# Kernel tuning notes

Measured on AMD Instinct MI355X. Metric: run time of the kernel, lower is better.

## Reference

```python
import jax, jax.numpy as jnp
import numpy as np

N_NODES = 100000
N_EDGES = 1600000
N_GRAPHS = 256
IN_DIM, HID, OUT_DIM = 20, 128, 30954


def setup_inputs() -> dict:
    key = jax.random.key(0)
    ks = jax.random.split(key, 9)
    x = jax.random.normal(ks[0], (N_NODES, IN_DIM), dtype=jnp.float32)
    edge_index = jax.random.randint(ks[1], (2, N_EDGES), 0, N_NODES, dtype=jnp.int64)
    batch = jnp.sort(jax.random.randint(ks[2], (N_NODES,), 0, N_GRAPHS, dtype=jnp.int64))
    s = 0.05
    W1 = jax.random.normal(ks[3], (IN_DIM, HID), dtype=jnp.float32) * s
    b1 = jax.random.normal(ks[4], (HID,), dtype=jnp.float32) * s
    W2 = jax.random.normal(ks[5], (HID, HID), dtype=jnp.float32) * s
    b2 = jax.random.normal(ks[6], (HID,), dtype=jnp.float32) * s
    Wc = jax.random.normal(ks[7], (HID, OUT_DIM), dtype=jnp.float32) * s
    bc = jax.random.normal(ks[8], (OUT_DIM,), dtype=jnp.float32) * s
    return {"x": x, "edge_index": edge_index, "batch": batch,
            "W1": W1, "b1": b1, "W2": W2, "b2": b2, "Wc": Wc, "bc": bc}


def _gcn_norm(edge_index, n_nodes):
    # add self loops (PyG GCNConv default), symmetric normalization
    loops = jnp.arange(n_nodes, dtype=edge_index.dtype)
    src = jnp.concatenate([edge_index[0], loops])
    dst = jnp.concatenate([edge_index[1], loops])
    deg = jax.ops.segment_sum(jnp.ones_like(dst, dtype=jnp.float32), dst,
                              num_segments=n_nodes)
    dinv = jnp.where(deg > 0, jax.lax.rsqrt(deg), 0.0)
    norm = dinv[src] * dinv[dst]  # [E+N]
    return src, dst, norm


def _gcn_conv(x, src, dst, norm, W, b, n_nodes):
    h = x @ W                              # [N, out] transform first (fewer msg flops)
    msg = h[src] * norm[:, None]           # gather + scale
    out = jax.ops.segment_sum(msg, dst, num_segments=n_nodes)
    return out + b


def reference(x, edge_index, batch, W1, b1, W2, b2, Wc, bc):
    n = x.shape[0]
    src, dst, norm = _gcn_norm(edge_index, n)
    h = jax.nn.relu(_gcn_conv(x, src, dst, norm, W1, b1, n))
    # dropout is identity in eval mode
    h = jax.nn.relu(_gcn_conv(h, src, dst, norm, W2, b2, n))
    # global mean pool per graph
    sums = jax.ops.segment_sum(h, batch, num_segments=N_GRAPHS)       # [G, HID]
    cnts = jax.ops.segment_sum(jnp.ones((n,), jnp.float32), batch,
                               num_segments=N_GRAPHS)
    pooled = sums / jnp.maximum(cnts, 1.0)[:, None]
    return pooled @ Wc + bc  # [G, OUT_DIM]
```

## Files before the change

kernel.cpp:

```cpp
#include <hip/hip_runtime.h>

#define HID 128
#define SCAN_B 256

__device__ __forceinline__ float bf_lo(unsigned int u) { return __uint_as_float(u << 16); }
__device__ __forceinline__ float bf_hi(unsigned int u) { return __uint_as_float(u & 0xFFFF0000u); }
__device__ __forceinline__ unsigned short f2bf(float f) {
    unsigned int u = __float_as_uint(f);
    unsigned int r = (u + 0x7FFFu + ((u >> 16) & 1u)) >> 16;
    return (unsigned short)r;
}

__global__ void detect_kernel(const unsigned int* __restrict__ p, int* __restrict__ flag) {
    if (threadIdx.x == 0 && blockIdx.x == 0) {
        int is64 = 1;
        for (int i = 0; i < 64; ++i) {
            if (p[2 * i + 1] != 0u) { is64 = 0; break; }
        }
        *flag = is64;
    }
}

__global__ void cvtdeg_kernel(const void* __restrict__ p, int* __restrict__ out,
                              int* __restrict__ deg, int E, const int* __restrict__ flag) {
    int i = blockIdx.x * blockDim.x + threadIdx.x;
    if (i < 2 * E) {
        int v = (*flag) ? (int)((const long long*)p)[i] : ((const int*)p)[i];
        out[i] = v;
        if (i >= E) atomicAdd(&deg[v], 1);
    }
}

__global__ void zero_kernel(float4* __restrict__ p, long long n4) {
    long long i = (long long)blockIdx.x * blockDim.x + threadIdx.x;
    long long stride = (long long)gridDim.x * blockDim.x;
    for (; i < n4; i += stride) p[i] = make_float4(0.f, 0.f, 0.f, 0.f);
}

__global__ void cvtx_kernel(const float* __restrict__ x, unsigned short* __restrict__ xb, int n) {
    int i = blockIdx.x * blockDim.x + threadIdx.x;
    if (i < n) xb[i] = f2bf(x[i]);
}

__global__ __launch_bounds__(SCAN_B) void scan1_kernel(const int* __restrict__ deg,
                                                       int* __restrict__ incl,
                                                       int* __restrict__ blockSums, int N) {
    __shared__ int s[SCAN_B];
    int i = blockIdx.x * SCAN_B + threadIdx.x;
    int v = (i < N) ? deg[i] : 0;
    s[threadIdx.x] = v;
    __syncthreads();
#pragma unroll
    for (int off = 1; off < SCAN_B; off <<= 1) {
        int t = (threadIdx.x >= off) ? s[threadIdx.x - off] : 0;
        __syncthreads();
        s[threadIdx.x] += t;
        __syncthreads();
    }
    if (i < N) incl[i] = s[threadIdx.x];
    if (threadIdx.x == SCAN_B - 1) blockSums[blockIdx.x] = s[SCAN_B - 1];
}

__global__ __launch_bounds__(1024) void scan2_kernel(int* __restrict__ blockSums, int nb) {
    __shared__ int s[1024];
    int v = (threadIdx.x < nb) ? blockSums[threadIdx.x] : 0;
    s[threadIdx.x] = v;
    __syncthreads();
#pragma unroll
    for (int off = 1; off < 1024; off <<= 1) {
        int t = (threadIdx.x >= off) ? s[threadIdx.x - off] : 0;
        __syncthreads();
        s[threadIdx.x] += t;
        __syncthreads();
    }
    if (threadIdx.x < nb) blockSums[threadIdx.x] = (threadIdx.x > 0) ? s[threadIdx.x - 1] : 0;
}

__global__ void scan3_kernel(const int* __restrict__ incl, const int* __restrict__ deg,
                             const int* __restrict__ blockSums, int* __restrict__ rowstart,
                             float* __restrict__ dinv, int* __restrict__ cursor,
                             int N, int E) {
    int i = blockIdx.x * blockDim.x + threadIdx.x;
    if (i < N) {
        int d = deg[i];
        rowstart[i] = incl[i] - d + blockSums[i / SCAN_B];
        dinv[i] = rsqrtf((float)(d + 1));
        cursor[i] = 0;
    }
    if (i == 0) rowstart[N] = E;
}

__global__ void scatter_kernel(const int* __restrict__ src, const int* __restrict__ dst,
                               const int* __restrict__ rowstart, int* __restrict__ cursor,
                               int2* __restrict__ elist, const float* __restrict__ dinv, int E) {
    int e = blockIdx.x * blockDim.x + threadIdx.x;
    if (e >= E) return;
    int s = src[e], d = dst[e];
    int pos = rowstart[d] + atomicAdd(&cursor[d], 1);
    float nm = dinv[s] * dinv[d];
    elist[pos] = make_int2(s, __float_as_int(nm));
}

__global__ void gstart_kernel(const void* __restrict__ bt, const int* __restrict__ flag,
                              int* __restrict__ gstart, int N, int G) {
    int g = blockIdx.x * blockDim.x + threadIdx.x;
    if (g > G) return;
    int is64 = *flag;
    int lo = 0, hi = N;
    while (lo < hi) {
        int mid = (lo + hi) >> 1;
        int v = is64 ? (int)((const long long*)bt)[mid] : ((const int*)bt)[mid];
        if (v < g) lo = mid + 1; else hi = mid;
    }
    gstart[g] = lo;
}

__global__ __launch_bounds__(256) void agg_lin1_kernel(const float* __restrict__ x,
                                                       const unsigned short* __restrict__ xb,
                                                       const float* __restrict__ W,
                                                       const float* __restrict__ b,
                                                       float* __restrict__ h,
                                                       const int* __restrict__ rowstart,
                                                       const int2* __restrict__ elist,
                                                       const float* __restrict__ dinv,
                                                       int N, int IN) {
    __shared__ float Ws[20 * HID];
    __shared__ float zs[8][20];
    const int tid = threadIdx.x;
    for (int i = tid; i < IN * HID; i += 256) Ws[i] = W[i];

    const int g = tid >> 5;
    const int j = tid & 31;
    const int node = blockIdx.x * 8 + g;
    const bool act = (node < N) && (j < IN);

    if (node < N) {
        int beg = rowstart[node], end = rowstart[node + 1];
        float acc = 0.f;
        int e = beg;
        for (; e + 1 < end; e += 2) {
            int2 p0 = elist[e];
            int2 p1 = elist[e + 1];
            float v0 = act ? bf_lo((unsigned int)xb[(size_t)p0.x * IN + j]) : 0.f;
            float v1 = act ? bf_lo((unsigned int)xb[(size_t)p1.x * IN + j]) : 0.f;
            acc += v0 * __int_as_float(p0.y);
            acc += v1 * __int_as_float(p1.y);
        }
        if (e < end) {
            int2 p0 = elist[e];
            if (act) acc += bf_lo((unsigned int)xb[(size_t)p0.x * IN + j]) * __int_as_float(p0.y);
        }
        if (act) {
            float di = dinv[node];
            zs[g][j] = acc + x[(size_t)node * IN + j] * di * di;
        }
    }
    __syncthreads();

    if (node < N) {
        float4 acc4 = ((const float4*)b)[j];
        for (int k = 0; k < IN; ++k) {
            float zv = zs[g][k];
            float4 w = *(const float4*)&Ws[k * HID + j * 4];
            acc4.x += zv * w.x; acc4.y += zv * w.y;
            acc4.z += zv * w.z; acc4.w += zv * w.w;
        }
        acc4.x = fmaxf(acc4.x, 0.f); acc4.y = fmaxf(acc4.y, 0.f);
        acc4.z = fmaxf(acc4.z, 0.f); acc4.w = fmaxf(acc4.w, 0.f);
        ((float4*)h)[(size_t)node * 32 + j] = acc4;
    }
}

#define TBM 64
#define TBN 64
#define TBK 32
#define XLD (TBM + 4)

__global__ __launch_bounds__(256) void gemm128_kernel(const float* __restrict__ A,
                                                      const float* __restrict__ W,
                                                      unsigned short* __restrict__ Cb, int N) {
    __shared__ float xs[TBK][XLD];
    __shared__ float wsh[TBK][TBN + 4];
    const int tid = threadIdx.x;
    const int n0 = blockIdx.x * TBM;
    const int c0 = blockIdx.y * TBN;
    const int ng = tid >> 4;
    const int cg = tid & 15;
    const int anode = tid >> 3;
    const int af    = tid & 7;
    const int wk    = tid >> 4;
    const int wc    = tid & 15;

    float acc[4][4] = {};

    for (int k0 = 0; k0 < HID; k0 += TBK) {
#pragma unroll
        for (int r = 0; r < 2; ++r) {
            int node = anode + r * 32;
            int gn = n0 + node;
            float4 v = make_float4(0.f, 0.f, 0.f, 0.f);
            if (gn < N) v = *(const float4*)(A + (size_t)gn * HID + k0 + af * 4);
            xs[af * 4 + 0][node] = v.x;
            xs[af * 4 + 1][node] = v.y;
            xs[af * 4 + 2][node] = v.z;
            xs[af * 4 + 3][node] = v.w;
        }
#pragma unroll
        for (int r = 0; r < 2; ++r) {
            int kk = wk + r * 16;
            *(float4*)&wsh[kk][wc * 4] =
                *(const float4*)(W + (size_t)(k0 + kk) * HID + c0 + wc * 4);
        }
        __syncthreads();
#pragma unroll
        for (int kk = 0; kk < TBK; ++kk) {
            float a[4], b[4];
            *(float4*)a = *(const float4*)&xs[kk][ng * 4];
            *(float4*)b = *(const float4*)&wsh[kk][cg * 4];
#pragma unroll
            for (int m = 0; m < 4; ++m)
#pragma unroll
                for (int n = 0; n < 4; ++n) acc[m][n] += a[m] * b[n];
        }
        __syncthreads();
    }

#pragma unroll
    for (int m = 0; m < 4; ++m) {
        int gn = n0 + ng * 4 + m;
        if (gn < N) {
            ushort4 st;
            st.x = f2bf(acc[m][0]); st.y = f2bf(acc[m][1]);
            st.z = f2bf(acc[m][2]); st.w = f2bf(acc[m][3]);
            *(ushort4*)(Cb + (size_t)gn * HID + c0 + cg * 4) = st;
        }
    }
}

__global__ __launch_bounds__(256) void csr_aggb_kernel(const unsigned short* __restrict__ h2b,
                                                       float* __restrict__ outb,
                                                       const int* __restrict__ rowstart,
                                                       const int2* __restrict__ elist,
                                                       const float* __restrict__ dinv,
                                                       const float* __restrict__ bias,
                                                       int N) {
    int node = blockIdx.x * 16 + (threadIdx.x >> 4);
    if (node >= N) return;
    int q = threadIdx.x & 15;
    const uint4* hv = (const uint4*)h2b;
    float acc[8] = {};
    int beg = rowstart[node], end = rowstart[node + 1];
    int e = beg;
    for (; e + 1 < end; e += 2) {
        int2 p0 = elist[e];
        int2 p1 = elist[e + 1];
        uint4 a0 = hv[(size_t)p0.x * 16 + q];
        uint4 a1 = hv[(size_t)p1.x * 16 + q];
        float n0 = __int_as_float(p0.y), n1 = __int_as_float(p1.y);
        acc[0] += bf_lo(a0.x) * n0 + bf_lo(a1.x) * n1;
        acc[1] += bf_hi(a0.x) * n0 + bf_hi(a1.x) * n1;
        acc[2] += bf_lo(a0.y) * n0 + bf_lo(a1.y) * n1;
        acc[3] += bf_hi(a0.y) * n0 + bf_hi(a1.y) * n1;
        acc[4] += bf_lo(a0.z) * n0 + bf_lo(a1.z) * n1;
        acc[5] += bf_hi(a0.z) * n0 + bf_hi(a1.z) * n1;
        acc[6] += bf_lo(a0.w) * n0 + bf_lo(a1.w) * n1;
        acc[7] += bf_hi(a0.w) * n0 + bf_hi(a1.w) * n1;
    }
    if (e < end) {
        int2 p0 = elist[e];
        uint4 a0 = hv[(size_t)p0.x * 16 + q];
        float n0 = __int_as_float(p0.y);
        acc[0] += bf_lo(a0.x) * n0; acc[1] += bf_hi(a0.x) * n0;
        acc[2] += bf_lo(a0.y) * n0; acc[3] += bf_hi(a0.y) * n0;
        acc[4] += bf_lo(a0.z) * n0; acc[5] += bf_hi(a0.z) * n0;
        acc[6] += bf_lo(a0.w) * n0; acc[7] += bf_hi(a0.w) * n0;
    }
    float di = dinv[node];
    float dd = di * di;
    uint4 sv = hv[(size_t)node * 16 + q];
    float self[8] = { bf_lo(sv.x), bf_hi(sv.x), bf_lo(sv.y), bf_hi(sv.y),
                      bf_lo(sv.z), bf_hi(sv.z), bf_lo(sv.w), bf_hi(sv.w) };
    float4 b0 = ((const float4*)bias)[2 * q];
    float4 b1 = ((const float4*)bias)[2 * q + 1];
    float4 r0, r1;
    r0.x = fmaxf(acc[0] + self[0] * dd + b0.x, 0.f);
    r0.y = fmaxf(acc[1] + self[1] * dd + b0.y, 0.f);
    r0.z = fmaxf(acc[2] + self[2] * dd + b0.z, 0.f);
    r0.w = fmaxf(acc[3] + self[3] * dd + b0.w, 0.f);
    r1.x = fmaxf(acc[4] + self[4] * dd + b1.x, 0.f);
    r1.y = fmaxf(acc[5] + self[5] * dd + b1.y, 0.f);
    r1.z = fmaxf(acc[6] + self[6] * dd + b1.z, 0.f);
    r1.w = fmaxf(acc[7] + self[7] * dd + b1.w, 0.f);
    ((float4*)outb)[(size_t)node * 32 + 2 * q] = r0;
    ((float4*)outb)[(size_t)node * 32 + 2 * q + 1] = r1;
}

__global__ __launch_bounds__(1024) void pool2_kernel(const float* __restrict__ h,
                                                     const int* __restrict__ gstart,
                                                     float* __restrict__ meanp, int G) {
    int g = blockIdx.x;
    int part = threadIdx.x >> 7;
    int j = threadIdx.x & 127;
    int beg = gstart[g], end = gstart[g + 1];
    float s = 0.f;
    for (int n = beg + part; n < end; n += 8) s += h[(size_t)n * HID + j];
    __shared__ float red[8][HID];
    red[part][j] = s;
    __syncthreads();
    if (part == 0) {
        float tot = 0.f;
#pragma unroll
        for (int r = 0; r < 8; ++r) tot += red[r][j];
        float c = (float)(end - beg);
        meanp[(size_t)g * HID + j] = tot / fmaxf(c, 1.f);
    }
}

#define CBM 64
#define CBN 64
#define CBK 32

__global__ __launch_bounds__(256) void clsgemm_kernel(const float* __restrict__ A,
                                                      const float* __restrict__ Bw,
                                                      const float* __restrict__ bc,
                                                      float* __restrict__ C,
                                                      int G, int OUT) {
    __shared__ float as[CBK][CBM + 4];
    __shared__ float bs[CBK][CBN + 4];
    const int tid = threadIdx.x;
    const int g0 = blockIdx.y * CBM;
    const int c0 = blockIdx.x * CBN;
    const int mg = tid >> 4;
    const int cg = tid & 15;
    const int arow = tid >> 3;
    const int af   = tid & 7;
    const int wk   = tid >> 4;
    const int wc   = tid & 15;

    float acc[4][4] = {};

    for (int k0 = 0; k0 < HID; k0 += CBK) {
#pragma unroll
        for (int r = 0; r < 2; ++r) {
            int row = arow + r * 32;
            int g = g0 + row;
            float4 v = make_float4(0.f, 0.f, 0.f, 0.f);
            if (g < G) v = *(const float4*)(A + (size_t)g * HID + k0 + af * 4);
            as[af * 4 + 0][row] = v.x;
            as[af * 4 + 1][row] = v.y;
            as[af * 4 + 2][row] = v.z;
            as[af * 4 + 3][row] = v.w;
        }
#pragma unroll
        for (int r = 0; r < 2; ++r) {
            int kk = wk + r * 16;
            int c = c0 + wc * 4;
            const float* bp = Bw + (size_t)(k0 + kk) * OUT + c;
            float2 lo = make_float2(0.f, 0.f), hi = make_float2(0.f, 0.f);
            if (c + 3 < OUT) {
                lo = *(const float2*)bp;
                hi = *(const float2*)(bp + 2);
            } else {
                if (c + 0 < OUT) lo.x = bp[0];
                if (c + 1 < OUT) lo.y = bp[1];
                if (c + 2 < OUT) hi.x = bp[2];
                if (c + 3 < OUT) hi.y = bp[3];
            }
            bs[kk][wc * 4 + 0] = lo.x;
            bs[kk][wc * 4 + 1] = lo.y;
            bs[kk][wc * 4 + 2] = hi.x;
            bs[kk][wc * 4 + 3] = hi.y;
        }
        __syncthreads();
#pragma unroll
        for (int kk = 0; kk < CBK; ++kk) {
            float a[4], b[4];
            *(float4*)a = *(const float4*)&as[kk][mg * 4];
            *(float4*)b = *(const float4*)&bs[kk][cg * 4];
#pragma unroll
            for (int m = 0; m < 4; ++m)
#pragma unroll
                for (int n = 0; n < 4; ++n) acc[m][n] += a[m] * b[n];
        }
        __syncthreads();
    }

    int c = c0 + cg * 4;
    float b0 = (c + 0 < OUT) ? bc[c + 0] : 0.f;
    float b1 = (c + 1 < OUT) ? bc[c + 1] : 0.f;
    float b2 = (c + 2 < OUT) ? bc[c + 2] : 0.f;
    float b3 = (c + 3 < OUT) ? bc[c + 3] : 0.f;
#pragma unroll
    for (int m = 0; m < 4; ++m) {
        int g = g0 + mg * 4 + m;
        if (g >= G) continue;
        float* cp = C + (size_t)g * OUT + c;
        if (c + 3 < OUT) {
            *(float2*)cp = make_float2(acc[m][0] + b0, acc[m][1] + b1);
            *(float2*)(cp + 2) = make_float2(acc[m][2] + b2, acc[m][3] + b3);
        } else {
            if (c + 0 < OUT) cp[0] = acc[m][0] + b0;
            if (c + 1 < OUT) cp[1] = acc[m][1] + b1;
            if (c + 2 < OUT) cp[2] = acc[m][2] + b2;
            if (c + 3 < OUT) cp[3] = acc[m][3] + b3;
        }
    }
}

extern "C" void kernel_launch(void* const* d_in, const int* in_sizes, int n_in,
                              void* d_out, int out_size, void* d_ws, size_t ws_size,
                              hipStream_t stream) {
    const float* x  = (const float*)d_in[0];
    const void*  ei = d_in[1];
    const void*  bt = d_in[2];
    const float* W1 = (const float*)d_in[3];
    const float* b1 = (const float*)d_in[4];
    const float* W2 = (const float*)d_in[5];
    const float* b2 = (const float*)d_in[6];
    const float* Wc = (const float*)d_in[7];
    const float* bc = (const float*)d_in[8];
    float* out = (float*)d_out;

    const int N   = in_sizes[2];
    const int E   = in_sizes[1] / 2;
    const int IN  = in_sizes[0] / N;
    const int OUT = in_sizes[8];
    const int G   = out_size / OUT;

    char* ws = (char*)d_ws;
    size_t off = 0;
    auto alloc = [&](size_t bytes) {
        size_t p = off;
        off += (bytes + 255) & ~(size_t)255;
        return p;
    };
    int*            idx32    = (int*)(ws + alloc((size_t)2 * E * 4));
    int*            deg      = (int*)(ws + alloc((size_t)N * 4));
    float*          dinv     = (float*)(ws + alloc((size_t)N * 4));
    int*            incl     = (int*)(ws + alloc((size_t)N * 4));
    int*            rowstart = (int*)(ws + alloc((size_t)(N + 1) * 4));
    int*            cursor   = (int*)(ws + alloc((size_t)N * 4));
    int*            blockSums= (int*)(ws + alloc((size_t)1024 * 4));
    int2*           elist    = (int2*)(ws + alloc((size_t)E * 8));
    unsigned short* xb       = (unsigned short*)(ws + alloc((size_t)N * IN * 2));
    float*          bufA     = (float*)(ws + alloc((size_t)N * HID * 4));
    unsigned short* h2b      = (unsigned short*)(ws + alloc((size_t)N * HID * 2));
    int*            gstart   = (int*)(ws + alloc((size_t)(G + 1) * 4));
    float*          meanp    = (float*)(ws + alloc((size_t)G * HID * 4));
    int*            flag     = (int*)(ws + alloc(4));
    (void)ws_size;

    int* srcI = idx32;
    int* dstI = idx32 + E;

    const int B = 256;
    const int nb = (N + SCAN_B - 1) / SCAN_B;

    detect_kernel<<<1, 64, 0, stream>>>((const unsigned int*)ei, flag);
    zero_kernel<<<256, B, 0, stream>>>((float4*)deg, (long long)N / 4);
    cvtdeg_kernel<<<(2 * E + B - 1) / B, B, 0, stream>>>(ei, idx32, deg, E, flag);
    cvtx_kernel<<<(N * IN + B - 1) / B, B, 0, stream>>>(x, xb, N * IN);

    scan1_kernel<<<nb, SCAN_B, 0, stream>>>(deg, incl, blockSums, N);
    scan2_kernel<<<1, 1024, 0, stream>>>(blockSums, nb);
    scan3_kernel<<<(N + B - 1) / B, B, 0, stream>>>(incl, deg, blockSums, rowstart,
                                                    dinv, cursor, N, E);
    scatter_kernel<<<(E + B - 1) / B, B, 0, stream>>>(srcI, dstI, rowstart, cursor, elist, dinv, E);

    gstart_kernel<<<2, 256, 0, stream>>>(bt, flag, gstart, N, G);

    agg_lin1_kernel<<<(N + 7) / 8, 256, 0, stream>>>(x, xb, W1, b1, bufA, rowstart, elist,
                                                     dinv, N, IN);

    {
        dim3 grid((N + TBM - 1) / TBM, HID / TBN);
        gemm128_kernel<<<grid, 256, 0, stream>>>(bufA, W2, h2b, N);
    }
    csr_aggb_kernel<<<(N + 15) / 16, 256, 0, stream>>>(h2b, bufA, rowstart, elist, dinv, b2, N);

    pool2_kernel<<<G, 1024, 0, stream>>>(bufA, gstart, meanp, G);

    {
        dim3 grid((OUT + CBN - 1) / CBN, (G + CBM - 1) / CBM);
        clsgemm_kernel<<<grid, 256, 0, stream>>>(meanp, Wc, bc, out, G, OUT);
    }
}
```

Before: 420.7 us.

## Pack bf16 pairs in layer-1 gather, unroll layer-2 gather, store bf16 activations

The layer-1 aggregation now reads two bf16 features per 32-bit load and splits each node's edges across two half-warps, combining them with a shuffle. This doubles useful lanes and halves the number of gather loads. The layer-2 CSR aggregation is unrolled to four edges per iteration to keep more loads in flight. Its ReLU output is stored as bf16 and read back by the pooling kernel, halving that write/read traffic at the cost of extra rounding before the mean pool.

```diff
diff --git a/kernel.cpp b/kernel.cpp
--- a/kernel.cpp
+++ b/kernel.cpp
@@ -116,7 +116,7 @@
 }
 
 __global__ __launch_bounds__(256) void agg_lin1_kernel(const float* __restrict__ x,
-                                                       const unsigned short* __restrict__ xb,
+                                                       const unsigned int* __restrict__ xb32,
                                                        const float* __restrict__ W,
                                                        const float* __restrict__ b,
                                                        float* __restrict__ h,
@@ -129,35 +129,47 @@
     const int tid = threadIdx.x;
     for (int i = tid; i < IN * HID; i += 256) Ws[i] = W[i];
 
-    const int g = tid >> 5;
-    const int j = tid & 31;
-    const int node = blockIdx.x * 8 + g;
-    const bool act = (node < N) && (j < IN);
-
+    const int g      = tid >> 5;
+    const int lane32 = tid & 31;
+    const int slot   = lane32 >> 4;
+    const int l      = lane32 & 15;
+    const int node   = blockIdx.x * 8 + g;
+    const int half   = IN >> 1;
+    const bool act   = (node < N) && (l < half);
+
+    float accx = 0.f, accy = 0.f;
     if (node < N) {
         int beg = rowstart[node], end = rowstart[node + 1];
-        float acc = 0.f;
-        int e = beg;
-        for (; e + 1 < end; e += 2) {
+        int e = beg + slot;
+        for (; e + 2 < end; e += 4) {
             int2 p0 = elist[e];
-            int2 p1 = elist[e + 1];
-            float v0 = act ? bf_lo((unsigned int)xb[(size_t)p0.x * IN + j]) : 0.f;
-            float v1 = act ? bf_lo((unsigned int)xb[(size_t)p1.x * IN + j]) : 0.f;
-            acc += v0 * __int_as_float(p0.y);
-            acc += v1 * __int_as_float(p1.y);
+            int2 p1 = elist[e + 2];
+            unsigned int u0 = act ? xb32[(size_t)p0.x * half + l] : 0u;
+            unsigned int u1 = act ? xb32[(size_t)p1.x * half + l] : 0u;
+            float n0 = __int_as_float(p0.y), n1 = __int_as_float(p1.y);
+            accx += bf_lo(u0) * n0 + bf_lo(u1) * n1;
+            accy += bf_hi(u0) * n0 + bf_hi(u1) * n1;
         }
         if (e < end) {
             int2 p0 = elist[e];
-            if (act) acc += bf_lo((unsigned int)xb[(size_t)p0.x * IN + j]) * __int_as_float(p0.y);
-        }
-        if (act) {
-            float di = dinv[node];
-            zs[g][j] = acc + x[(size_t)node * IN + j] * di * di;
-        }
+            unsigned int u0 = act ? xb32[(size_t)p0.x * half + l] : 0u;
+            float n0 = __int_as_float(p0.y);
+            accx += bf_lo(u0) * n0;
+            accy += bf_hi(u0) * n0;
+        }
+    }
+    accx += __shfl_xor(accx, 16, 64);
+    accy += __shfl_xor(accy, 16, 64);
+    if (node < N && slot == 0 && l < half) {
+        float di = dinv[node];
+        float dd = di * di;
+        zs[g][2 * l]     = accx + x[(size_t)node * IN + 2 * l] * dd;
+        zs[g][2 * l + 1] = accy + x[(size_t)node * IN + 2 * l + 1] * dd;
     }
     __syncthreads();
 
     if (node < N) {
+        const int j = lane32;
         float4 acc4 = ((const float4*)b)[j];
         for (int k = 0; k < IN; ++k) {
             float zv = zs[g][k];
@@ -238,7 +250,7 @@
 }
 
 __global__ __launch_bounds__(256) void csr_aggb_kernel(const unsigned short* __restrict__ h2b,
-                                                       float* __restrict__ outb,
+                                                       unsigned short* __restrict__ outb,
                                                        const int* __restrict__ rowstart,
                                                        const int2* __restrict__ elist,
                                                        const float* __restrict__ dinv,
@@ -251,22 +263,27 @@
     float acc[8] = {};
     int beg = rowstart[node], end = rowstart[node + 1];
     int e = beg;
-    for (; e + 1 < end; e += 2) {
+    for (; e + 3 < end; e += 4) {
         int2 p0 = elist[e];
         int2 p1 = elist[e + 1];
+        int2 p2 = elist[e + 2];
+        int2 p3 = elist[e + 3];
         uint4 a0 = hv[(size_t)p0.x * 16 + q];
         uint4 a1 = hv[(size_t)p1.x * 16 + q];
+        uint4 a2 = hv[(size_t)p2.x * 16 + q];
+        uint4 a3 = hv[(size_t)p3.x * 16 + q];
         float n0 = __int_as_float(p0.y), n1 = __int_as_float(p1.y);
-        acc[0] += bf_lo(a0.x) * n0 + bf_lo(a1.x) * n1;
-        acc[1] += bf_hi(a0.x) * n0 + bf_hi(a1.x) * n1;
-        acc[2] += bf_lo(a0.y) * n0 + bf_lo(a1.y) * n1;
-        acc[3] += bf_hi(a0.y) * n0 + bf_hi(a1.y) * n1;
-        acc[4] += bf_lo(a0.z) * n0 + bf_lo(a1.z) * n1;
-        acc[5] += bf_hi(a0.z) * n0 + bf_hi(a1.z) * n1;
-        acc[6] += bf_lo(a0.w) * n0 + bf_lo(a1.w) * n1;
-        acc[7] += bf_hi(a0.w) * n0 + bf_hi(a1.w) * n1;
-    }
-    if (e < end) {
+        float n2 = __int_as_float(p2.y), n3 = __int_as_float(p3.y);
+        acc[0] += bf_lo(a0.x) * n0 + bf_lo(a1.x) * n1 + bf_lo(a2.x) * n2 + bf_lo(a3.x) * n3;
+        acc[1] += bf_hi(a0.x) * n0 + bf_hi(a1.x) * n1 + bf_hi(a2.x) * n2 + bf_hi(a3.x) * n3;
+        acc[2] += bf_lo(a0.y) * n0 + bf_lo(a1.y) * n1 + bf_lo(a2.y) * n2 + bf_lo(a3.y) * n3;
+        acc[3] += bf_hi(a0.y) * n0 + bf_hi(a1.y) * n1 + bf_hi(a2.y) * n2 + bf_hi(a3.y) * n3;
+        acc[4] += bf_lo(a0.z) * n0 + bf_lo(a1.z) * n1 + bf_lo(a2.z) * n2 + bf_lo(a3.z) * n3;
+        acc[5] += bf_hi(a0.z) * n0 + bf_hi(a1.z) * n1 + bf_hi(a2.z) * n2 + bf_hi(a3.z) * n3;
+        acc[6] += bf_lo(a0.w) * n0 + bf_lo(a1.w) * n1 + bf_lo(a2.w) * n2 + bf_lo(a3.w) * n3;
+        acc[7] += bf_hi(a0.w) * n0 + bf_hi(a1.w) * n1 + bf_hi(a2.w) * n2 + bf_hi(a3.w) * n3;
+    }
+    for (; e < end; ++e) {
         int2 p0 = elist[e];
         uint4 a0 = hv[(size_t)p0.x * 16 + q];
         float n0 = __int_as_float(p0.y);
@@ -282,20 +299,24 @@
                       bf_lo(sv.z), bf_hi(sv.z), bf_lo(sv.w), bf_hi(sv.w) };
     float4 b0 = ((const float4*)bias)[2 * q];
     float4 b1 = ((const float4*)bias)[2 * q + 1];
-    float4 r0, r1;
-    r0.x = fmaxf(acc[0] + self[0] * dd + b0.x, 0.f);
-    r0.y = fmaxf(acc[1] + self[1] * dd + b0.y, 0.f);
-    r0.z = fmaxf(acc[2] + self[2] * dd + b0.z, 0.f);
-    r0.w = fmaxf(acc[3] + self[3] * dd + b0.w, 0.f);
-    r1.x = fmaxf(acc[4] + self[4] * dd + b1.x, 0.f);
-    r1.y = fmaxf(acc[5] + self[5] * dd + b1.y, 0.f);
-    r1.z = fmaxf(acc[6] + self[6] * dd + b1.z, 0.f);
-    r1.w = fmaxf(acc[7] + self[7] * dd + b1.w, 0.f);
-    ((float4*)outb)[(size_t)node * 32 + 2 * q] = r0;
-    ((float4*)outb)[(size_t)node * 32 + 2 * q + 1] = r1;
-}
-
-__global__ __launch_bounds__(1024) void pool2_kernel(const float* __restrict__ h,
+    float r[8];
+    r[0] = fmaxf(acc[0] + self[0] * dd + b0.x, 0.f);
+    r[1] = fmaxf(acc[1] + self[1] * dd + b0.y, 0.f);
+    r[2] = fmaxf(acc[2] + self[2] * dd + b0.z, 0.f);
+    r[3] = fmaxf(acc[3] + self[3] * dd + b0.w, 0.f);
+    r[4] = fmaxf(acc[4] + self[4] * dd + b1.x, 0.f);
+    r[5] = fmaxf(acc[5] + self[5] * dd + b1.y, 0.f);
+    r[6] = fmaxf(acc[6] + self[6] * dd + b1.z, 0.f);
+    r[7] = fmaxf(acc[7] + self[7] * dd + b1.w, 0.f);
+    uint4 st;
+    st.x = (unsigned)f2bf(r[0]) | ((unsigned)f2bf(r[1]) << 16);
+    st.y = (unsigned)f2bf(r[2]) | ((unsigned)f2bf(r[3]) << 16);
+    st.z = (unsigned)f2bf(r[4]) | ((unsigned)f2bf(r[5]) << 16);
+    st.w = (unsigned)f2bf(r[6]) | ((unsigned)f2bf(r[7]) << 16);
+    ((uint4*)outb)[(size_t)node * 16 + q] = st;
+}
+
+__global__ __launch_bounds__(1024) void pool2_kernel(const unsigned short* __restrict__ hb,
                                                      const int* __restrict__ gstart,
                                                      float* __restrict__ meanp, int G) {
     int g = blockIdx.x;
@@ -303,7 +324,8 @@
     int j = threadIdx.x & 127;
     int beg = gstart[g], end = gstart[g + 1];
     float s = 0.f;
-    for (int n = beg + part; n < end; n += 8) s += h[(size_t)n * HID + j];
+    for (int n = beg + part; n < end; n += 8)
+        s += __uint_as_float(((unsigned)hb[(size_t)n * HID + j]) << 16);
     __shared__ float red[8][HID];
     red[part][j] = s;
     __syncthreads();
@@ -452,6 +474,7 @@
 
     int* srcI = idx32;
     int* dstI = idx32 + E;
+    unsigned short* houtb = (unsigned short*)bufA;
 
     const int B = 256;
     const int nb = (N + SCAN_B - 1) / SCAN_B;
@@ -469,16 +492,16 @@
 
     gstart_kernel<<<2, 256, 0, stream>>>(bt, flag, gstart, N, G);
 
-    agg_lin1_kernel<<<(N + 7) / 8, 256, 0, stream>>>(x, xb, W1, b1, bufA, rowstart, elist,
-                                                     dinv, N, IN);
+    agg_lin1_kernel<<<(N + 7) / 8, 256, 0, stream>>>(x, (const unsigned int*)xb, W1, b1,
+                                                     bufA, rowstart, elist, dinv, N, IN);
 
     {
         dim3 grid((N + TBM - 1) / TBM, HID / TBN);
         gemm128_kernel<<<grid, 256, 0, stream>>>(bufA, W2, h2b, N);
     }
-    csr_aggb_kernel<<<(N + 15) / 16, 256, 0, stream>>>(h2b, bufA, rowstart, elist, dinv, b2, N);
-
-    pool2_kernel<<<G, 1024, 0, stream>>>(bufA, gstart, meanp, G);
+    csr_aggb_kernel<<<(N + 15) / 16, 256, 0, stream>>>(h2b, houtb, rowstart, elist, dinv, b2, N);
+
+    pool2_kernel<<<G, 1024, 0, stream>>>(houtb, gstart, meanp, G);
 
     {
         dim3 grid((OUT + CBN - 1) / CBN, (G + CBM - 1) / CBM);
```

New measurement: 385.0 us. -8.5%, faster.
